# Performance work log

Measured on AMD Instinct MI355X. Metric: run time of the kernel, lower is better.

## Reference

```python
import jax, jax.numpy as jnp
import numpy as np

DIM = 512
HEADS = 8
DHEAD = DIM // 8          # 64
INNER = HEADS * DHEAD     # 512
M = DIM // 2              # 256 landmarks
ITERS = 6                 # pinv iterations
SCALE = DHEAD ** -0.5
LN_EPS = 1e-5             # torch LayerNorm default
KCONV = 33                # residual_conv_kernel default


def setup_inputs() -> dict:
    key = jax.random.key(0)
    ks = jax.random.split(key, 5)
    B, N = 2, 4096
    x = jax.random.normal(ks[0], (B, N, DIM), jnp.float32)
    ln_w = jnp.ones((DIM,), jnp.float32)
    ln_b = jnp.zeros((DIM,), jnp.float32)
    qkv_w = jax.random.normal(ks[1], (3 * INNER, DIM), jnp.float32) * 0.02
    out_w = jax.random.normal(ks[2], (DIM, INNER), jnp.float32) * 0.02
    out_b = jnp.zeros((DIM,), jnp.float32)
    conv_w = jax.random.normal(ks[3], (HEADS, 1, KCONV, 1), jnp.float32) * 0.05
    return dict(x=x, ln_w=ln_w, ln_b=ln_b, qkv_w=qkv_w,
                out_w=out_w, out_b=out_b, conv_w=conv_w)


def moore_penrose_pinv(x, iters=ITERS):
    # faithful to lucidrains: global (scalar) max over row/col abs-sums
    abs_x = jnp.abs(x)
    z = jnp.swapaxes(x, -1, -2) / (jnp.max(abs_x.sum(-1)) * jnp.max(abs_x.sum(-2)))
    I = jnp.eye(x.shape[-1], dtype=x.dtype)
    for _ in range(iters):
        xz = x @ z
        z = 0.25 * z @ (13 * I - xz @ (15 * I - xz @ (7 * I - xz)))
    return z


def reference(x, ln_w, ln_b, qkv_w, out_w, out_b, conv_w):
    B, N, D = x.shape
    # LayerNorm
    mu = x.mean(-1, keepdims=True)
    var = ((x - mu) ** 2).mean(-1, keepdims=True)
    xn = (x - mu) / jnp.sqrt(var + LN_EPS) * ln_w + ln_b
    # qkv projection (N divisible by M -> no padding branch)
    qkv = xn @ qkv_w.T                                   # [B,N,3*INNER]
    q, k, v = jnp.split(qkv, 3, axis=-1)

    def to_heads(t):
        return t.reshape(B, N, HEADS, DHEAD).transpose(0, 2, 1, 3)  # [B,H,N,Dh]

    q, k, v = to_heads(q), to_heads(k), to_heads(v)
    q = q * SCALE
    l = N // M  # tokens per landmark
    q_land = q.reshape(B, HEADS, M, l, DHEAD).mean(3)    # [B,H,M,Dh]
    k_land = k.reshape(B, HEADS, M, l, DHEAD).mean(3)
    sim1 = jnp.einsum('bhid,bhjd->bhij', q, k_land)      # [B,H,N,M]
    sim2 = jnp.einsum('bhid,bhjd->bhij', q_land, k_land) # [B,H,M,M]
    sim3 = jnp.einsum('bhid,bhjd->bhij', q_land, k)      # [B,H,M,N]
    a1 = jax.nn.softmax(sim1, -1)
    a2 = jax.nn.softmax(sim2, -1)
    a3 = jax.nn.softmax(sim3, -1)
    a2_inv = moore_penrose_pinv(a2)
    out = (a1 @ a2_inv) @ (a3 @ v)                       # [B,H,N,Dh]
    # depthwise residual conv on v along sequence (kernel 33, pad 16)
    res = jax.lax.conv_general_dilated(
        v, conv_w, window_strides=(1, 1),
        padding=((KCONV // 2, KCONV // 2), (0, 0)),
        dimension_numbers=('NCHW', 'OIHW', 'NCHW'),
        feature_group_count=HEADS)
    out = out + res
    out = out.transpose(0, 2, 1, 3).reshape(B, N, INNER)
    attn_out = out @ out_w.T + out_b                     # dropout = eval identity
    return x + attn_out
```

## Files before the change

kernel.cpp:

```cpp
#include <hip/hip_runtime.h>
#include <math.h>

#define DIMD  512
#define NSEQ  4096
#define BATCH 2
#define HEADS 8
#define DHEAD 64
#define MLAND 256
#define BH    (BATCH*HEADS)
#define QSCALE 0.125f
#define LN_EPS 1e-5f
#define KCONV 33

typedef __attribute__((ext_vector_type(8))) short bf16x8;
typedef __attribute__((ext_vector_type(4))) float f32x4;

#define WB(p, mb) ((char*)(p) + (size_t)(mb) * 1048576ull)

__device__ __forceinline__ unsigned short f2b(float f) {
  unsigned u = __float_as_uint(f);
  return (unsigned short)((u + 0x7FFFu + ((u >> 16) & 1u)) >> 16);
}
__device__ __forceinline__ float b2f(unsigned short h) {
  return __uint_as_float(((unsigned)h) << 16);
}

__device__ __forceinline__ float block_red(float v, float* s4, bool sum) {
#pragma unroll
  for (int o = 32; o; o >>= 1) {
    float t = __shfl_xor(v, o);
    v = sum ? v + t : fmaxf(v, t);
  }
  int wid = threadIdx.x >> 6;
  if ((threadIdx.x & 63) == 0) s4[wid] = v;
  __syncthreads();
  float r = sum ? (s4[0] + s4[1] + s4[2] + s4[3])
                : fmaxf(fmaxf(s4[0], s4[1]), fmaxf(s4[2], s4[3]));
  __syncthreads();
  return r;
}

__device__ __forceinline__ void gload16(const unsigned short* g, short* lds) {
  __builtin_amdgcn_global_load_lds(
      (const __attribute__((address_space(1))) void*)g,
      (__attribute__((address_space(3))) void*)lds, 16, 0, 0);
}

template<int ROWS>
__device__ __forceinline__ void stage_lds(const unsigned short* __restrict__ g, int ld,
                                          short* lds, int tid) {
  int l = tid & 63, w = tid >> 6;
  int r_in = l >> 2, c8 = (l & 3) * 8;
  constexpr int PER = ROWS / 64;
#pragma unroll
  for (int p = 0; p < PER; ++p) {
    int r0 = (w * PER + p) * 16;
    gload16(g + (size_t)(r0 + r_in) * ld + c8, lds + r0 * 32);
  }
}

__device__ __forceinline__ void mma_step32(const short* As, const short* Bs,
                                           int wrow, int wcol, int l, f32x4 acc[4][4]) {
  int lr = l & 15, lk = (l >> 4) * 8;
  bf16x8 af[4], bf_[4];
#pragma unroll
  for (int f = 0; f < 4; ++f) {
    af[f]  = *(const bf16x8*)&As[(wrow + f * 16 + lr) * 32 + lk];
    bf_[f] = *(const bf16x8*)&Bs[(wcol + f * 16 + lr) * 32 + lk];
  }
#pragma unroll
  for (int i = 0; i < 4; ++i)
#pragma unroll
    for (int j = 0; j < 4; ++j)
      acc[i][j] = __builtin_amdgcn_mfma_f32_16x16x32_bf16(af[i], bf_[j], acc[i][j], 0, 0, 0);
}


__global__ void k_init(unsigned* scal) {
  if (threadIdx.x < 4) scal[threadIdx.x] = 0u;
}

__global__ __launch_bounds__(256) void k_ln_wconv(const float* __restrict__ x,
                                                  const float* __restrict__ w,
                                                  const float* __restrict__ b,
                                                  const float* __restrict__ qkvw,
                                                  const float* __restrict__ outw,
                                                  unsigned short* __restrict__ xnh,
                                                  unsigned short* __restrict__ wqh,
                                                  unsigned short* __restrict__ owh) {
  if (blockIdx.x >= 2048) {
    int idx = (blockIdx.x - 2048) * 256 + threadIdx.x;
    if (idx < 786432) wqh[idx] = f2b(qkvw[idx]);
    else owh[idx - 786432] = f2b(outw[idx - 786432]);
    return;
  }
  int lane = threadIdx.x & 63;
  int row = blockIdx.x * 4 + (threadIdx.x >> 6);
  const float* xr = x + (size_t)row * DIMD;
  float4 v0 = *(const float4*)&xr[lane * 8];
  float4 v1 = *(const float4*)&xr[lane * 8 + 4];
  float s  = v0.x + v0.y + v0.z + v0.w + v1.x + v1.y + v1.z + v1.w;
  float ss = v0.x*v0.x + v0.y*v0.y + v0.z*v0.z + v0.w*v0.w
           + v1.x*v1.x + v1.y*v1.y + v1.z*v1.z + v1.w*v1.w;
#pragma unroll
  for (int o = 32; o; o >>= 1) { s += __shfl_xor(s, o); ss += __shfl_xor(ss, o); }
  float mu = s * (1.f / 512.f);
  float var = ss * (1.f / 512.f) - mu * mu;
  float rstd = rsqrtf(var + LN_EPS);
  float4 w0 = *(const float4*)&w[lane * 8];
  float4 w1 = *(const float4*)&w[lane * 8 + 4];
  float4 b0 = *(const float4*)&b[lane * 8];
  float4 b1 = *(const float4*)&b[lane * 8 + 4];
  float o0x = (v0.x - mu) * rstd * w0.x + b0.x;
  float o0y = (v0.y - mu) * rstd * w0.y + b0.y;
  float o0z = (v0.z - mu) * rstd * w0.z + b0.z;
  float o0w = (v0.w - mu) * rstd * w0.w + b0.w;
  float o1x = (v1.x - mu) * rstd * w1.x + b1.x;
  float o1y = (v1.y - mu) * rstd * w1.y + b1.y;
  float o1z = (v1.z - mu) * rstd * w1.z + b1.z;
  float o1w = (v1.w - mu) * rstd * w1.w + b1.w;
  uint4 pk;
  pk.x = (unsigned)f2b(o0x) | ((unsigned)f2b(o0y) << 16);
  pk.y = (unsigned)f2b(o0z) | ((unsigned)f2b(o0w) << 16);
  pk.z = (unsigned)f2b(o1x) | ((unsigned)f2b(o1y) << 16);
  pk.w = (unsigned)f2b(o1z) | ((unsigned)f2b(o1w) << 16);
  *(uint4*)&xnh[(size_t)row * DIMD + lane * 8] = pk;
}

__global__ __launch_bounds__(256) void k_qkv_mfma(const unsigned short* __restrict__ xnh,
                                                  const unsigned short* __restrict__ wqh,
                                                  unsigned short* __restrict__ qh,
                                                  unsigned short* __restrict__ kh,
                                                  unsigned short* __restrict__ vh,
                                                  unsigned short* __restrict__ vTh) {
  __shared__ short As[128 * 32], Bs[128 * 32];
  int tid = threadIdx.x, l = tid & 63, wid = tid >> 6;
  int wrow = (wid >> 1) * 64, wcol = (wid & 1) * 64;
  int m0 = blockIdx.y * 128, c0 = blockIdx.x * 128;
  f32x4 acc[4][4] = {};
  for (int k0 = 0; k0 < 512; k0 += 32) {
    __syncthreads();
    stage_lds<128>(xnh + (size_t)m0 * 512 + k0, 512, As, tid);
    stage_lds<128>(wqh + (size_t)c0 * 512 + k0, 512, Bs, tid);
    __syncthreads();
    mma_step32(As, Bs, wrow, wcol, l, acc);
  }
  const int which = c0 >> 9;
#pragma unroll
  for (int i = 0; i < 4; ++i) {
#pragma unroll
    for (int j = 0; j < 4; ++j) {
      int col = c0 + wcol + j * 16 + (l & 15);
      int hh = (col >> 6) & 7, d = col & 63;
      int m_base = m0 + wrow + i * 16 + ((l >> 4) * 4);
      int bb = m_base >> 12, n0 = m_base & 4095;
      size_t hb = (size_t)(bb * 8 + hh);
      if (which == 0) {
#pragma unroll
        for (int r = 0; r < 4; ++r)
          qh[(hb * 4096 + n0 + r) * 64 + d] = f2b(acc[i][j][r] * QSCALE);
      } else if (which == 1) {
#pragma unroll
        for (int r = 0; r < 4; ++r)
          kh[(hb * 4096 + n0 + r) * 64 + d] = f2b(acc[i][j][r]);
      } else {
        ushort4 hv;
        hv.x = f2b(acc[i][j][0]); hv.y = f2b(acc[i][j][1]);
        hv.z = f2b(acc[i][j][2]); hv.w = f2b(acc[i][j][3]);
#pragma unroll
        for (int r = 0; r < 4; ++r)
          vh[(hb * 4096 + n0 + r) * 64 + d] = (&hv.x)[r];
        *(ushort4*)&vTh[(hb * 64 + d) * 4096 + n0] = hv;
      }
    }
  }
}

__global__ __launch_bounds__(256) void k_land(const unsigned short* __restrict__ q,
                                              const unsigned short* __restrict__ k,
                                              float* __restrict__ ql,
                                              float* __restrict__ kl,
                                              unsigned short* __restrict__ qlh,
                                              unsigned short* __restrict__ klh) {
  int idx = blockIdx.x * 256 + threadIdx.x;
  int sel = idx >= (BH * MLAND * DHEAD);
  int e = sel ? idx - BH * MLAND * DHEAD : idx;
  int bh = e >> 14; int m = (e >> 6) & 255; int d = e & 63;
  const unsigned short* src = sel ? k : q;
  size_t base = ((size_t)bh * 4096 + m * 16) * 64 + d;
  float s = 0;
#pragma unroll
  for (int t = 0; t < 16; ++t) s += b2f(src[base + t * 64]);
  float val = s * (1.f / 16.f);
  (sel ? kl : ql)[e] = val;
  (sel ? klh : qlh)[e] = f2b(val);
}

__global__ __launch_bounds__(256) void k_sim2(const float* __restrict__ ql,
                                              const float* __restrict__ kl,
                                              float* __restrict__ a2,
                                              unsigned short* __restrict__ a2h) {
  __shared__ float qs[64];
  __shared__ float s4[4];
  int i = blockIdx.x, bh = blockIdx.y, tid = threadIdx.x;
  if (tid < 16) ((float4*)qs)[tid] = ((const float4*)(ql + ((size_t)bh * 256 + i) * 64))[tid];
  __syncthreads();
  const float* kr = kl + ((size_t)bh * 256 + tid) * 64;
  float s = 0;
#pragma unroll
  for (int d = 0; d < 64; d += 4) {
    float4 kv = *(const float4*)&kr[d];
    s += qs[d] * kv.x + qs[d + 1] * kv.y + qs[d + 2] * kv.z + qs[d + 3] * kv.w;
  }
  float mx = block_red(s, s4, false);
  float p = expf(s - mx);
  float tot = block_red(p, s4, true);
  float val = p / tot;
  a2[((size_t)bh * 256 + i) * 256 + tid] = val;
  a2h[((size_t)bh * 256 + i) * 256 + tid] = f2b(val);
}

__global__ __launch_bounds__(256) void k_pinv_red(const float* __restrict__ a2,
                                                  unsigned* __restrict__ scal) {
  __shared__ float s4[4];
  int bh = blockIdx.x, tid = threadIdx.x;
  const float* m = a2 + (size_t)bh * 65536;
  float cs = 0;
  for (int i = 0; i < 256; ++i) cs += fabsf(m[(size_t)i * 256 + tid]);
  float rs = 0;
  const float* row = m + (size_t)tid * 256;
  for (int j = 0; j < 256; j += 4) {
    float4 v = *(const float4*)&row[j];
    rs += fabsf(v.x) + fabsf(v.y) + fabsf(v.z) + fabsf(v.w);
  }
  float mc = block_red(cs, s4, false);
  float mr = block_red(rs, s4, false);
  if (tid == 0) {
    atomicMax(&scal[0], __float_as_uint(mr));
    atomicMax(&scal[1], __float_as_uint(mc));
  }
}

__global__ __launch_bounds__(256) void k_z0h(const float* __restrict__ a2,
                                             const unsigned* __restrict__ scal,
                                             unsigned short* __restrict__ zh,
                                             unsigned short* __restrict__ zTh) {
  int idx = blockIdx.x * 256 + threadIdx.x;
  float inv = 1.f / (__uint_as_float(scal[0]) * __uint_as_float(scal[1]));
  int bh = idx >> 16, r = (idx >> 8) & 255, c = idx & 255;
  zh[idx]  = f2b(a2[((size_t)bh << 16) + (c << 8) + r] * inv);
  zTh[idx] = f2b(a2[idx] * inv);
}

__global__ __launch_bounds__(256) void k_pg2(const unsigned short* __restrict__ A,
                                             const unsigned short* __restrict__ Bsrc,
                                             unsigned short* __restrict__ C,
                                             unsigned short* __restrict__ CT,
                                             float g, float bI, float s) {
  __shared__ short As[8 * 64 * 32], Bs[8 * 64 * 32];
  int tid = threadIdx.x, l = tid & 63, w = tid >> 6;
  int bh = blockIdx.x & 15, t = blockIdx.x >> 4;
  int i0 = (t >> 2) * 64, j0 = (t & 3) * 64;
  A += (size_t)bh * 65536; Bsrc += (size_t)bh * 65536;

#pragma unroll
  for (int ks = 0; ks < 8; ++ks)
    stage_lds<64>(A + (size_t)i0 * 256 + ks * 32, 256, As + ks * 2048, tid);

#pragma unroll
  for (int u = tid; u < 2048; u += 256) {
    int r = u >> 5, q8 = u & 31;
    int ks = q8 >> 2, p = q8 & 3;
    uint4 vv = *(const uint4*)(Bsrc + (size_t)(j0 + r) * 256 + q8 * 8);
    unsigned short* e = (unsigned short*)&vv;
    int n = j0 + r, kb = q8 * 8;
#pragma unroll
    for (int q = 0; q < 8; ++q) {
      float f = b2f(e[q]) * g + ((n == kb + q) ? bI : 0.f);
      e[q] = f2b(f);
    }
    *(uint4*)(Bs + ks * 2048 + r * 32 + p * 8) = vv;
  }
  __syncthreads();

  int lr = l & 15, lk = (l >> 4) * 8;
  f32x4 acc[4] = {};
#pragma unroll
  for (int ks = 0; ks < 8; ++ks) {
    const short* Ac = As + ks * 2048;
    const short* Bc = Bs + ks * 2048;
    bf16x8 af = *(const bf16x8*)&Ac[(w * 16 + lr) * 32 + lk];
#pragma unroll
    for (int j = 0; j < 4; ++j) {
      bf16x8 bf_ = *(const bf16x8*)&Bc[(j * 16 + lr) * 32 + lk];
      acc[j] = __builtin_amdgcn_mfma_f32_16x16x32_bf16(af, bf_, acc[j], 0, 0, 0);
    }
  }

#pragma unroll
  for (int j = 0; j < 4; ++j) {
    int col = j0 + j * 16 + lr;
    int row0 = i0 + w * 16 + (l >> 4) * 4;
    ushort4 hv;
    hv.x = f2b(acc[j][0] * s); hv.y = f2b(acc[j][1] * s);
    hv.z = f2b(acc[j][2] * s); hv.w = f2b(acc[j][3] * s);
    if (CT) *(ushort4*)&CT[(size_t)bh * 65536 + (size_t)col * 256 + row0] = hv;
    if (C) {
      unsigned short* cb = C + (size_t)bh * 65536 + (size_t)row0 * 256 + col;
      cb[0] = hv.x; cb[256] = hv.y; cb[512] = hv.z; cb[768] = hv.w;
    }
  }
}

__global__ __launch_bounds__(256) void k_sim3_mfma(const unsigned short* __restrict__ qlh,
                                                   const unsigned short* __restrict__ kh,
                                                   unsigned short* __restrict__ sim3h) {
  __shared__ short As[128 * 32], Bs[128 * 32];
  int tid = threadIdx.x, l = tid & 63, wid = tid >> 6;
  int wrow = (wid >> 1) * 64, wcol = (wid & 1) * 64;
  int bh = blockIdx.z;
  int m0 = blockIdx.y * 128, n0 = blockIdx.x * 128;
  const unsigned short* A = qlh + (size_t)bh * 256 * 64;
  const unsigned short* B = kh + (size_t)bh * 4096 * 64;
  f32x4 acc[4][4] = {};
  for (int k0 = 0; k0 < 64; k0 += 32) {
    __syncthreads();
    stage_lds<128>(A + (size_t)m0 * 64 + k0, 64, As, tid);
    stage_lds<128>(B + (size_t)n0 * 64 + k0, 64, Bs, tid);
    __syncthreads();
    mma_step32(As, Bs, wrow, wcol, l, acc);
  }
  unsigned short* Cm = sim3h + (size_t)bh * 1048576;
#pragma unroll
  for (int i = 0; i < 4; ++i)
#pragma unroll
    for (int j = 0; j < 4; ++j) {
      int col = n0 + wcol + j * 16 + (l & 15);
      int row0 = m0 + wrow + i * 16 + (l >> 4) * 4;
#pragma unroll
      for (int r = 0; r < 4; ++r)
        Cm[(size_t)(row0 + r) * 4096 + col] = f2b(acc[i][j][r]);
    }
}

__global__ __launch_bounds__(256) void k_rowstat(const unsigned short* __restrict__ sim,
                                                 float* __restrict__ rs) {
  __shared__ float s4[4];
  int m = blockIdx.x, bh = blockIdx.y, tid = threadIdx.x;
  const unsigned short* row = sim + ((size_t)bh * 256 + m) * 4096;
  float v[16];
  float mx = -1e30f;
#pragma unroll
  for (int i = 0; i < 16; ++i) { v[i] = b2f(row[i * 256 + tid]); mx = fmaxf(mx, v[i]); }
  mx = block_red(mx, s4, false);
  float ssum = 0;
#pragma unroll
  for (int i = 0; i < 16; ++i) ssum += expf(v[i] - mx);
  ssum = block_red(ssum, s4, true);
  if (tid == 0) {
    rs[(size_t)(bh * 256 + m) * 2]     = mx;
    rs[(size_t)(bh * 256 + m) * 2 + 1] = 1.f / ssum;
  }
}

__global__ __launch_bounds__(256) void k_a3v_mfma(const unsigned short* __restrict__ a3h,
                                                  const unsigned short* __restrict__ vTh,
                                                  const float* __restrict__ rs,
                                                  float* __restrict__ part) {
  __shared__ short As[256 * 32], Bs[64 * 32];
  int tid = threadIdx.x, l = tid & 63, wid = tid >> 6;
  int wrow = wid * 64, wcol = 0;
  int kc = blockIdx.x, bh = blockIdx.z;
  const unsigned short* A = a3h + (size_t)bh * 1048576 + kc * 256;
  const unsigned short* B = vTh + (size_t)bh * 262144 + kc * 256;
  rs += (size_t)bh * 512;
  const int rA = tid >> 2, cA8 = (tid & 3) * 8;
  f32x4 acc[4][4] = {};
  uint4 pre[4];
#pragma unroll
  for (int p = 0; p < 4; ++p)
    pre[p] = *(const uint4*)(A + (size_t)(rA + 64 * p) * 4096 + cA8);
#pragma unroll 1
  for (int ks = 0; ks < 8; ++ks) {
    __syncthreads();
#pragma unroll
    for (int p = 0; p < 4; ++p) {
      int r = rA + 64 * p;
      uint4 vv = pre[p];
      unsigned short* e = (unsigned short*)&vv;
      float m_ = rs[r * 2], inv_ = rs[r * 2 + 1];
#pragma unroll
      for (int q = 0; q < 8; ++q)
        e[q] = f2b(expf(b2f(e[q]) - m_) * inv_);
      *(uint4*)(As + r * 32 + cA8) = vv;
    }
    stage_lds<64>(B + ks * 32, 4096, Bs, tid);
    __syncthreads();
    if (ks < 7) {
#pragma unroll
      for (int p = 0; p < 4; ++p)
        pre[p] = *(const uint4*)(A + (size_t)(rA + 64 * p) * 4096 + (ks + 1) * 32 + cA8);
    }
    mma_step32(As, Bs, wrow, wcol, l, acc);
  }
  float* P = part + ((size_t)(kc * 16 + bh)) * 16384;
#pragma unroll
  for (int i = 0; i < 4; ++i)
#pragma unroll
    for (int j = 0; j < 4; ++j) {
      int col = j * 16 + (l & 15);
      int row0 = wrow + i * 16 + (l >> 4) * 4;
#pragma unroll
      for (int r = 0; r < 4; ++r)
        P[(size_t)(row0 + r) * 64 + col] = acc[i][j][r];
    }
}

__global__ __launch_bounds__(256) void k_a3v_redT(const float* __restrict__ part,
                                                  unsigned short* __restrict__ a3vT) {
  int idx = blockIdx.x * 256 + threadIdx.x;
  int d = idx & 63, m = (idx >> 6) & 255, bh = idx >> 14;
  float s = 0;
#pragma unroll
  for (int c = 0; c < 16; ++c) s += part[((size_t)(c * 16 + bh) * 256 + m) * 64 + d];
  a3vT[(size_t)bh * 16384 + d * 256 + m] = f2b(s);
}

__global__ __launch_bounds__(256) void k_wm_mfma(const unsigned short* __restrict__ zh,
                                                 const unsigned short* __restrict__ a3vTh,
                                                 unsigned short* __restrict__ wmTh) {
  __shared__ short As[256 * 32], Bs[64 * 32];
  int tid = threadIdx.x, l = tid & 63, wid = tid >> 6;
  int wrow = wid * 64, wcol = 0;
  int bh = blockIdx.z;
  const unsigned short* A = zh + (size_t)bh * 65536;
  const unsigned short* B = a3vTh + (size_t)bh * 16384;
  f32x4 acc[4][4] = {};
  for (int k0 = 0; k0 < 256; k0 += 32) {
    __syncthreads();
    stage_lds<256>(A + k0, 256, As, tid);
    stage_lds<64>(B + k0, 256, Bs, tid);
    __syncthreads();
    mma_step32(As, Bs, wrow, wcol, l, acc);
  }
  unsigned short* W = wmTh + (size_t)bh * 16384;
#pragma unroll
  for (int i = 0; i < 4; ++i)
#pragma unroll
    for (int j = 0; j < 4; ++j) {
      int col = j * 16 + (l & 15);
      int row0 = wrow + i * 16 + (l >> 4) * 4;
#pragma unroll
      for (int r = 0; r < 4; ++r)
        W[(size_t)col * 256 + row0 + r] = f2b(acc[i][j][r]);
    }
}

#define FSM_Q    0
#define FSM_KL   16384
#define FSM_WMT  0
#define FSM_P    32768
#define FSM_OUT  0
#define FSM_V    32768
__global__ __launch_bounds__(512) void k_fused_mfma(const unsigned short* __restrict__ qh,
                                                    const unsigned short* __restrict__ klh,
                                                    const unsigned short* __restrict__ wmTh,
                                                    const unsigned short* __restrict__ vh,
                                                    const float* __restrict__ cw,
                                                    unsigned short* __restrict__ yh) {
  __shared__ char sm[55808];
  int tid = threadIdx.x, l = tid & 63, w = tid >> 6;
  int h = blockIdx.y, b = blockIdx.z, bh = b * HEADS + h;
  int n0 = blockIdx.x * 128;
  const char* qg = (const char*)(qh + ((size_t)bh * 4096 + n0) * 64);
  const char* kg = (const char*)(klh + (size_t)bh * 256 * 64);

#pragma unroll
  for (int u = tid; u < 1024; u += 512) {
    int row = u >> 3, cb = (u & 7) * 16;
    *(uint4*)(sm + FSM_Q + row * 128 + (cb ^ ((row & 7) << 4))) =
        *(const uint4*)(qg + row * 128 + cb);
  }
#pragma unroll
  for (int u = tid; u < 2048; u += 512) {
    int row = u >> 3, cb = (u & 7) * 16;
    *(uint4*)(sm + FSM_KL + row * 128 + (cb ^ ((row & 7) << 4))) =
        *(const uint4*)(kg + row * 128 + cb);
  }
  __syncthreads();

  int lr = l & 15, lkb = (l >> 4) * 16;
  int arow = 16 * w + lr;
  int aswz = (arow & 7) << 4;
  f32x4 acc[16] = {};
#pragma unroll
  for (int ks = 0; ks < 2; ++ks) {
    bf16x8 af = *(const bf16x8*)(sm + FSM_Q + arow * 128 + ((ks * 64 + lkb) ^ aswz));
#pragma unroll
    for (int j = 0; j < 16; ++j) {
      int brow = j * 16 + lr;
      bf16x8 bf_ = *(const bf16x8*)(sm + FSM_KL + brow * 128 + ((ks * 64 + lkb) ^ ((brow & 7) << 4)));
      acc[j] = __builtin_amdgcn_mfma_f32_16x16x32_bf16(af, bf_, acc[j], 0, 0, 0);
    }
  }

#pragma unroll
  for (int r = 0; r < 4; ++r) {
    float mx = -1e30f;
#pragma unroll
    for (int j = 0; j < 16; ++j) mx = fmaxf(mx, acc[j][r]);
#pragma unroll
    for (int o = 8; o; o >>= 1) mx = fmaxf(mx, __shfl_xor(mx, o));
    float s = 0.f;
#pragma unroll
    for (int j = 0; j < 16; ++j) { float e = expf(acc[j][r] - mx); acc[j][r] = e; s += e; }
#pragma unroll
    for (int o = 8; o; o >>= 1) s += __shfl_xor(s, o);
    float inv = 1.f / s;
#pragma unroll
    for (int j = 0; j < 16; ++j) acc[j][r] *= inv;
  }
  __syncthreads();

  const char* wg = (const char*)(wmTh + (size_t)bh * 16384);
#pragma unroll
  for (int u = tid; u < 2048; u += 512) {
    int row = u >> 5, cb = (u & 31) * 16;
    *(uint4*)(sm + FSM_WMT + row * 512 + (cb ^ ((row & 7) << 4))) =
        *(const uint4*)(wg + row * 512 + cb);
  }

  f32x4 acc2[4] = {};
  int prow0 = 16 * w + (l >> 4) * 4;
#pragma unroll
  for (int mc = 0; mc < 4; ++mc) {
    __syncthreads();
#pragma unroll
    for (int j2 = 0; j2 < 4; ++j2)
#pragma unroll
      for (int r = 0; r < 4; ++r) {
        int row = prow0 + r;
        int colb = (j2 * 16 + lr) * 2;
        *(unsigned short*)(sm + FSM_P + row * 128 + (colb ^ ((row & 7) << 4))) =
            f2b(acc[mc * 4 + j2][r]);
      }
    __syncthreads();
#pragma unroll
    for (int ks = 0; ks < 2; ++ks) {
      bf16x8 af = *(const bf16x8*)(sm + FSM_P + arow * 128 + ((ks * 64 + lkb) ^ aswz));
#pragma unroll
      for (int j = 0; j < 4; ++j) {
        int brow = j * 16 + lr;
        bf16x8 bf_ = *(const bf16x8*)(sm + FSM_WMT + brow * 512 +
                                      ((mc * 128 + ks * 64 + lkb) ^ ((brow & 7) << 4)));
        acc2[j] = __builtin_amdgcn_mfma_f32_16x16x32_bf16(af, bf_, acc2[j], 0, 0, 0);
      }
    }
  }
  __syncthreads();

#pragma unroll
  for (int j = 0; j < 4; ++j)
#pragma unroll
    for (int r = 0; r < 4; ++r)
      *(float*)(sm + FSM_OUT + (prow0 + r) * 256 + (j * 16 + lr) * 4) = acc2[j][r];

  const char* vg = (const char*)(vh + (size_t)bh * 4096 * 64);
#pragma unroll
  for (int u = tid; u < 1280; u += 512) {
    int row = u >> 3, cb = (u & 7) * 16;
    int n = n0 - 16 + row;
    uint4 vv; vv.x = 0; vv.y = 0; vv.z = 0; vv.w = 0;
    if (n >= 0 && n < 4096) vv = *(const uint4*)(vg + (size_t)n * 128 + cb);
    *(uint4*)(sm + FSM_V + row * 144 + cb) = vv;
  }
  __syncthreads();

#pragma unroll
  for (int u = tid; u < 1024; u += 512) {
    int row = u >> 3, d8 = (u & 7) * 8;
    float r8[8] = {};
#pragma unroll 1
    for (int t = 0; t < KCONV; ++t) {
      float wt = cw[h * KCONV + t];
      ushort4 a0 = *(const ushort4*)(sm + FSM_V + (row + t) * 144 + d8 * 2);
      ushort4 a1 = *(const ushort4*)(sm + FSM_V + (row + t) * 144 + d8 * 2 + 8);
      r8[0] += wt * b2f(a0.x); r8[1] += wt * b2f(a0.y);
      r8[2] += wt * b2f(a0.z); r8[3] += wt * b2f(a0.w);
      r8[4] += wt * b2f(a1.x); r8[5] += wt * b2f(a1.y);
      r8[6] += wt * b2f(a1.z); r8[7] += wt * b2f(a1.w);
    }
    const float* ol = (const float*)(sm + FSM_OUT + row * 256 + d8 * 4);
    ushort4 s0, s1;
    s0.x = f2b(r8[0] + ol[0]); s0.y = f2b(r8[1] + ol[1]);
    s0.z = f2b(r8[2] + ol[2]); s0.w = f2b(r8[3] + ol[3]);
    s1.x = f2b(r8[4] + ol[4]); s1.y = f2b(r8[5] + ol[5]);
    s1.z = f2b(r8[6] + ol[6]); s1.w = f2b(r8[7] + ol[7]);
    unsigned short* yp = yh + ((size_t)b * 4096 + n0 + row) * 512 + h * 64 + d8;
    *(ushort4*)yp = s0;
    *(ushort4*)(yp + 4) = s1;
  }
}

__global__ __launch_bounds__(256) void k_outproj_mfma(const unsigned short* __restrict__ yh,
                                                      const unsigned short* __restrict__ owh,
                                                      const float* __restrict__ bias,
                                                      const float* __restrict__ x,
                                                      float* __restrict__ out) {
  __shared__ short As[128 * 32], Bs[128 * 32];
  int tid = threadIdx.x, l = tid & 63, wid = tid >> 6;
  int wrow = (wid >> 1) * 64, wcol = (wid & 1) * 64;
  int m0 = blockIdx.y * 128, c0 = blockIdx.x * 128;
  f32x4 acc[4][4] = {};
  for (int k0 = 0; k0 < 512; k0 += 32) {
    __syncthreads();
    stage_lds<128>(yh + (size_t)m0 * 512 + k0, 512, As, tid);
    stage_lds<128>(owh + (size_t)c0 * 512 + k0, 512, Bs, tid);
    __syncthreads();
    mma_step32(As, Bs, wrow, wcol, l, acc);
  }
#pragma unroll
  for (int i = 0; i < 4; ++i)
#pragma unroll
    for (int j = 0; j < 4; ++j) {
      int col = c0 + wcol + j * 16 + (l & 15);
      int row0 = m0 + wrow + i * 16 + (l >> 4) * 4;
      float bb = bias[col];
#pragma unroll
      for (int r = 0; r < 4; ++r) {
        size_t o = (size_t)(row0 + r) * 512 + col;
        out[o] = acc[i][j][r] + x[o] + bb;
      }
    }
}

extern "C" void kernel_launch(void* const* d_in, const int* in_sizes, int n_in,
                              void* d_out, int out_size, void* d_ws, size_t ws_size,
                              hipStream_t stream) {
  const float* x      = (const float*)d_in[0];
  const float* ln_w   = (const float*)d_in[1];
  const float* ln_b   = (const float*)d_in[2];
  const float* qkv_w  = (const float*)d_in[3];
  const float* out_w  = (const float*)d_in[4];
  const float* out_b  = (const float*)d_in[5];
  const float* conv_w = (const float*)d_in[6];
  float* out = (float*)d_out;

  unsigned short* vh  = (unsigned short*)WB(d_ws, 0);
  float* part = (float*)WB(d_ws, 12);
  float* ql   = (float*)WB(d_ws, 48);
  float* kl   = (float*)WB(d_ws, 49);
  float* a2   = (float*)WB(d_ws, 50);
  float* rs   = (float*)WB(d_ws, 62);
  unsigned* scal = (unsigned*)WB(d_ws, 63);
  unsigned short* xnh  = (unsigned short*)WB(d_ws, 64);
  unsigned short* wqh  = (unsigned short*)WB(d_ws, 72);
  unsigned short* owh  = (unsigned short*)WB(d_ws, 74);
  unsigned short* kh   = (unsigned short*)WB(d_ws, 76);
  unsigned short* vTh  = (unsigned short*)WB(d_ws, 84);
  unsigned short* qlh  = (unsigned short*)WB(d_ws, 92);
  unsigned short* a2h  = (unsigned short*)WB(d_ws, 93);
  unsigned short* zA   = (unsigned short*)WB(d_ws, 95);
  unsigned short* zAT  = (unsigned short*)WB(d_ws, 97);
  unsigned short* zB   = (unsigned short*)WB(d_ws, 99);
  unsigned short* zBT  = (unsigned short*)WB(d_ws, 101);
  unsigned short* Am   = (unsigned short*)WB(d_ws, 103);
  unsigned short* AmT  = (unsigned short*)WB(d_ws, 105);
  unsigned short* W2T  = (unsigned short*)WB(d_ws, 107);
  unsigned short* W4T  = (unsigned short*)WB(d_ws, 109);
  unsigned short* sim3h= (unsigned short*)WB(d_ws, 111);
  unsigned short* a3vTh= (unsigned short*)WB(d_ws, 143);
  unsigned short* yh   = (unsigned short*)WB(d_ws, 144);
  unsigned short* qhb  = (unsigned short*)WB(d_ws, 152);
  unsigned short* klhb = (unsigned short*)WB(d_ws, 168);
  unsigned short* wmTh = (unsigned short*)WB(d_ws, 169);

  k_init<<<1, 64, 0, stream>>>(scal);
  k_ln_wconv<<<6144, 256, 0, stream>>>(x, ln_w, ln_b, qkv_w, out_w, xnh, wqh, owh);
  k_qkv_mfma<<<dim3(12, 64), 256, 0, stream>>>(xnh, wqh, qhb, kh, vh, vTh);
  k_land<<<2048, 256, 0, stream>>>(qhb, kh, ql, kl, qlh, klhb);
  k_sim2<<<dim3(256, 16), 256, 0, stream>>>(ql, kl, a2, a2h);
  k_pinv_red<<<16, 256, 0, stream>>>(a2, scal);
  k_z0h<<<4096, 256, 0, stream>>>(a2, scal, zA, zAT);

  unsigned short *zc = zA, *zcT = zAT, *zn = zB, *znT = zBT;
  for (int it = 0; it < 6; ++it) {
    k_pg2<<<256, 256, 0, stream>>>(a2h, zcT, Am, AmT, 1.f, 0.f, 1.f);
    k_pg2<<<256, 256, 0, stream>>>(Am, AmT, (unsigned short*)nullptr, W2T, -1.f, 7.f, 1.f);
    k_pg2<<<256, 256, 0, stream>>>(Am, W2T, (unsigned short*)nullptr, W4T, -1.f, 15.f, 1.f);
    k_pg2<<<256, 256, 0, stream>>>(zc, W4T, zn, znT, -1.f, 13.f, 0.25f);
    unsigned short* t;
    t = zc; zc = zn; zn = t;
    t = zcT; zcT = znT; znT = t;
  }

  k_sim3_mfma<<<dim3(32, 2, 16), 256, 0, stream>>>(qlh, kh, sim3h);
  k_rowstat<<<dim3(256, 16), 256, 0, stream>>>(sim3h, rs);
  k_a3v_mfma<<<dim3(16, 1, 16), 256, 0, stream>>>(sim3h, vTh, rs, part);
  k_a3v_redT<<<1024, 256, 0, stream>>>(part, a3vTh);
  k_wm_mfma<<<dim3(1, 1, 16), 256, 0, stream>>>(zA, a3vTh, wmTh);
  k_fused_mfma<<<dim3(32, 8, 2), 512, 0, stream>>>(qhb, klhb, wmTh, vh, conv_w, yh);
  k_outproj_mfma<<<dim3(4, 64), 256, 0, stream>>>(yh, owh, out_b, x, out);
}
```

Before: 326.7 us.

## Deepen GEMM K-steps, split wm kernel across blocks, fold init into LN kernel

Several independent tweaks. The qkv and outproj GEMMs now stage 64-wide K chunks per barrier pair, halving the synchronisations. The sim3 kernel loads its full K=64 at once with a single barrier. The wm GEMM is re-tiled from 16 blocks to 64 blocks (4 row tiles per head) with all of K preloaded into LDS. The scalar-init kernel is removed, and its zeroing is folded into the LN/weight-convert kernel to save a launch. This costs more LDS per block, which may reduce occupancy.

New measurement: 315.8 us. -3.3%, faster.

```diff
diff --git a/kernel.cpp b/kernel.cpp
--- a/kernel.cpp
+++ b/kernel.cpp
@@ -76,10 +76,6 @@
 }
 
 
-__global__ void k_init(unsigned* scal) {
-  if (threadIdx.x < 4) scal[threadIdx.x] = 0u;
-}
-
 __global__ __launch_bounds__(256) void k_ln_wconv(const float* __restrict__ x,
                                                   const float* __restrict__ w,
                                                   const float* __restrict__ b,
@@ -87,11 +83,13 @@
                                                   const float* __restrict__ outw,
                                                   unsigned short* __restrict__ xnh,
                                                   unsigned short* __restrict__ wqh,
-                                                  unsigned short* __restrict__ owh) {
+                                                  unsigned short* __restrict__ owh,
+                                                  unsigned* __restrict__ scal) {
   if (blockIdx.x >= 2048) {
     int idx = (blockIdx.x - 2048) * 256 + threadIdx.x;
     if (idx < 786432) wqh[idx] = f2b(qkvw[idx]);
     else owh[idx - 786432] = f2b(outw[idx - 786432]);
+    if (blockIdx.x == 2048 && threadIdx.x < 4) scal[threadIdx.x] = 0u;
     return;
   }
   int lane = threadIdx.x & 63;
@@ -133,17 +131,20 @@
                                                   unsigned short* __restrict__ kh,
                                                   unsigned short* __restrict__ vh,
                                                   unsigned short* __restrict__ vTh) {
-  __shared__ short As[128 * 32], Bs[128 * 32];
+  __shared__ short As[2 * 128 * 32], Bs[2 * 128 * 32];
   int tid = threadIdx.x, l = tid & 63, wid = tid >> 6;
   int wrow = (wid >> 1) * 64, wcol = (wid & 1) * 64;
   int m0 = blockIdx.y * 128, c0 = blockIdx.x * 128;
   f32x4 acc[4][4] = {};
-  for (int k0 = 0; k0 < 512; k0 += 32) {
+  for (int k0 = 0; k0 < 512; k0 += 64) {
     __syncthreads();
     stage_lds<128>(xnh + (size_t)m0 * 512 + k0, 512, As, tid);
+    stage_lds<128>(xnh + (size_t)m0 * 512 + k0 + 32, 512, As + 4096, tid);
     stage_lds<128>(wqh + (size_t)c0 * 512 + k0, 512, Bs, tid);
+    stage_lds<128>(wqh + (size_t)c0 * 512 + k0 + 32, 512, Bs + 4096, tid);
     __syncthreads();
     mma_step32(As, Bs, wrow, wcol, l, acc);
+    mma_step32(As + 4096, Bs + 4096, wrow, wcol, l, acc);
   }
   const int which = c0 >> 9;
 #pragma unroll
@@ -315,7 +316,7 @@
 __global__ __launch_bounds__(256) void k_sim3_mfma(const unsigned short* __restrict__ qlh,
                                                    const unsigned short* __restrict__ kh,
                                                    unsigned short* __restrict__ sim3h) {
-  __shared__ short As[128 * 32], Bs[128 * 32];
+  __shared__ short As[2 * 128 * 32], Bs[2 * 128 * 32];
   int tid = threadIdx.x, l = tid & 63, wid = tid >> 6;
   int wrow = (wid >> 1) * 64, wcol = (wid & 1) * 64;
   int bh = blockIdx.z;
@@ -323,13 +324,13 @@
   const unsigned short* A = qlh + (size_t)bh * 256 * 64;
   const unsigned short* B = kh + (size_t)bh * 4096 * 64;
   f32x4 acc[4][4] = {};
-  for (int k0 = 0; k0 < 64; k0 += 32) {
-    __syncthreads();
-    stage_lds<128>(A + (size_t)m0 * 64 + k0, 64, As, tid);
-    stage_lds<128>(B + (size_t)n0 * 64 + k0, 64, Bs, tid);
-    __syncthreads();
-    mma_step32(As, Bs, wrow, wcol, l, acc);
-  }
+  stage_lds<128>(A + (size_t)m0 * 64, 64, As, tid);
+  stage_lds<128>(A + (size_t)m0 * 64 + 32, 64, As + 4096, tid);
+  stage_lds<128>(B + (size_t)n0 * 64, 64, Bs, tid);
+  stage_lds<128>(B + (size_t)n0 * 64 + 32, 64, Bs + 4096, tid);
+  __syncthreads();
+  mma_step32(As, Bs, wrow, wcol, l, acc);
+  mma_step32(As + 4096, Bs + 4096, wrow, wcol, l, acc);
   unsigned short* Cm = sim3h + (size_t)bh * 1048576;
 #pragma unroll
   for (int i = 0; i < 4; ++i)
@@ -429,31 +430,40 @@
 __global__ __launch_bounds__(256) void k_wm_mfma(const unsigned short* __restrict__ zh,
                                                  const unsigned short* __restrict__ a3vTh,
                                                  unsigned short* __restrict__ wmTh) {
-  __shared__ short As[256 * 32], Bs[64 * 32];
-  int tid = threadIdx.x, l = tid & 63, wid = tid >> 6;
-  int wrow = wid * 64, wcol = 0;
-  int bh = blockIdx.z;
-  const unsigned short* A = zh + (size_t)bh * 65536;
+  __shared__ short As[8 * 64 * 32], Bs[8 * 64 * 32];
+  int tid = threadIdx.x, l = tid & 63, w = tid >> 6;
+  int m0 = blockIdx.x * 64, bh = blockIdx.y;
+  const unsigned short* A = zh + (size_t)bh * 65536 + (size_t)m0 * 256;
   const unsigned short* B = a3vTh + (size_t)bh * 16384;
-  f32x4 acc[4][4] = {};
-  for (int k0 = 0; k0 < 256; k0 += 32) {
-    __syncthreads();
-    stage_lds<256>(A + k0, 256, As, tid);
-    stage_lds<64>(B + k0, 256, Bs, tid);
-    __syncthreads();
-    mma_step32(As, Bs, wrow, wcol, l, acc);
+#pragma unroll
+  for (int ks = 0; ks < 8; ++ks)
+    stage_lds<64>(A + ks * 32, 256, As + ks * 2048, tid);
+#pragma unroll
+  for (int ks = 0; ks < 8; ++ks)
+    stage_lds<64>(B + ks * 32, 256, Bs + ks * 2048, tid);
+  __syncthreads();
+  int lr = l & 15, lk = (l >> 4) * 8;
+  f32x4 acc[4] = {};
+#pragma unroll
+  for (int ks = 0; ks < 8; ++ks) {
+    const short* Ac = As + ks * 2048;
+    const short* Bc = Bs + ks * 2048;
+    bf16x8 af = *(const bf16x8*)&Ac[(w * 16 + lr) * 32 + lk];
+#pragma unroll
+    for (int j = 0; j < 4; ++j) {
+      bf16x8 bf_ = *(const bf16x8*)&Bc[(j * 16 + lr) * 32 + lk];
+      acc[j] = __builtin_amdgcn_mfma_f32_16x16x32_bf16(af, bf_, acc[j], 0, 0, 0);
+    }
   }
   unsigned short* W = wmTh + (size_t)bh * 16384;
 #pragma unroll
-  for (int i = 0; i < 4; ++i)
-#pragma unroll
-    for (int j = 0; j < 4; ++j) {
-      int col = j * 16 + (l & 15);
-      int row0 = wrow + i * 16 + (l >> 4) * 4;
-#pragma unroll
-      for (int r = 0; r < 4; ++r)
-        W[(size_t)col * 256 + row0 + r] = f2b(acc[i][j][r]);
-    }
+  for (int j = 0; j < 4; ++j) {
+    int col = j * 16 + lr;
+    int row0 = m0 + w * 16 + (l >> 4) * 4;
+#pragma unroll
+    for (int r = 0; r < 4; ++r)
+      W[(size_t)col * 256 + row0 + r] = f2b(acc[j][r]);
+  }
 }
 
 #define FSM_Q    0
@@ -607,17 +617,20 @@
                                                       const float* __restrict__ bias,
                                                       const float* __restrict__ x,
                                                       float* __restrict__ out) {
-  __shared__ short As[128 * 32], Bs[128 * 32];
+  __shared__ short As[2 * 128 * 32], Bs[2 * 128 * 32];
   int tid = threadIdx.x, l = tid & 63, wid = tid >> 6;
   int wrow = (wid >> 1) * 64, wcol = (wid & 1) * 64;
   int m0 = blockIdx.y * 128, c0 = blockIdx.x * 128;
   f32x4 acc[4][4] = {};
-  for (int k0 = 0; k0 < 512; k0 += 32) {
+  for (int k0 = 0; k0 < 512; k0 += 64) {
     __syncthreads();
     stage_lds<128>(yh + (size_t)m0 * 512 + k0, 512, As, tid);
+    stage_lds<128>(yh + (size_t)m0 * 512 + k0 + 32, 512, As + 4096, tid);
     stage_lds<128>(owh + (size_t)c0 * 512 + k0, 512, Bs, tid);
+    stage_lds<128>(owh + (size_t)c0 * 512 + k0 + 32, 512, Bs + 4096, tid);
     __syncthreads();
     mma_step32(As, Bs, wrow, wcol, l, acc);
+    mma_step32(As + 4096, Bs + 4096, wrow, wcol, l, acc);
   }
 #pragma unroll
   for (int i = 0; i < 4; ++i)
@@ -675,8 +688,7 @@
   unsigned short* klhb = (unsigned short*)WB(d_ws, 168);
   unsigned short* wmTh = (unsigned short*)WB(d_ws, 169);
 
-  k_init<<<1, 64, 0, stream>>>(scal);
-  k_ln_wconv<<<6144, 256, 0, stream>>>(x, ln_w, ln_b, qkv_w, out_w, xnh, wqh, owh);
+  k_ln_wconv<<<6144, 256, 0, stream>>>(x, ln_w, ln_b, qkv_w, out_w, xnh, wqh, owh, scal);
   k_qkv_mfma<<<dim3(12, 64), 256, 0, stream>>>(xnh, wqh, qhb, kh, vh, vTh);
   k_land<<<2048, 256, 0, stream>>>(qhb, kh, ql, kl, qlh, klhb);
   k_sim2<<<dim3(256, 16), 256, 0, stream>>>(ql, kl, a2, a2h);
@@ -698,7 +710,7 @@
   k_rowstat<<<dim3(256, 16), 256, 0, stream>>>(sim3h, rs);
   k_a3v_mfma<<<dim3(16, 1, 16), 256, 0, stream>>>(sim3h, vTh, rs, part);
   k_a3v_redT<<<1024, 256, 0, stream>>>(part, a3vTh);
-  k_wm_mfma<<<dim3(1, 1, 16), 256, 0, stream>>>(zA, a3vTh, wmTh);
+  k_wm_mfma<<<dim3(4, 16), 256, 0, stream>>>(zA, a3vTh, wmTh);
   k_fused_mfma<<<dim3(32, 8, 2), 512, 0, stream>>>(qhb, klhb, wmTh, vh, conv_w, yh);
   k_outproj_mfma<<<dim3(4, 64), 256, 0, stream>>>(yh, owh, out_b, x, out);
 }
```
